# Performance work log

Measured on AMD Instinct MI355X. Metric: run time of the kernel, lower is better.

Reference implementation:

```python
import jax, jax.numpy as jnp
import numpy as np

# FP4 E2M1 value table (codes 0..7 positive, 8..15 negative, sign in MSB)
FP4_VALUES = jnp.array([0.0, 0.5, 1.0, 1.5, 2.0, 3.0, 4.0, 6.0,
                        -0.0, -0.5, -1.0, -1.5, -2.0, -3.0, -4.0, -6.0],
                       dtype=jnp.float32)


def setup_inputs() -> dict:
    key = jax.random.key(0)
    k1, k2, k3, k4 = jax.random.split(key, 4)
    O, I = 4096, 4096
    block = 16
    x = jax.random.normal(k1, (8192, I), dtype=jnp.float32)
    # packed uint4 pairs stored as int32 bytes in [0, 256)
    weight = jax.random.randint(k2, (O, I // 2), 0, 256, dtype=jnp.int32)
    # per-block FP8-style scales (positive)
    weight_scale = jax.random.uniform(k3, (O, I // block), dtype=jnp.float32, minval=0.01, maxval=1.0)
    bias = jax.random.normal(k4, (O,), dtype=jnp.float32)
    return {"x": x, "weight": weight, "weight_scale": weight_scale,
            "bias": bias, "block_size": block}


def _dequant_nvfp4(weight, weight_scale, block_size):
    # unpack two FP4 codes per byte: high nibble is the even (first) element
    hi = (weight >> 4) & 0xF
    lo = weight & 0xF
    O = weight.shape[0]
    codes = jnp.stack([hi, lo], axis=-1).reshape(O, -1)  # [O, I]
    vals = FP4_VALUES[codes]                             # [O, I] f32
    I = vals.shape[1]
    # apply per-block scale
    w = vals.reshape(O, I // block_size, block_size) * weight_scale[:, :, None]
    return w.reshape(O, I)


def reference(x, weight, weight_scale, bias, block_size):
    w = _dequant_nvfp4(weight, weight_scale, block_size)  # [O, I]
    return jnp.einsum('ti,oi->to', x, w) + bias[None, :]
```

## Files before the change

kernel.cpp:

```cpp
#include <hip/hip_runtime.h>
#include <hip/hip_fp16.h>

typedef __attribute__((ext_vector_type(8))) _Float16 f16x8;
typedef __attribute__((ext_vector_type(4))) float f32x4;

#define M_DIM 8192
#define N_DIM 4096
#define K_DIM 4096
#define BM 256
#define BN 256
#define BK 64
#define NT (K_DIM / BK)
#define ITERS (NT / 2)

__constant__ float FP4_LUT[16] = {0.f, 0.5f, 1.f, 1.5f, 2.f, 3.f, 4.f, 6.f,
                                  -0.f, -0.5f, -1.f, -1.5f, -2.f, -3.f, -4.f, -6.f};

__device__ inline void glds16(const void* g, void* l) {
    __builtin_amdgcn_global_load_lds(
        (const __attribute__((address_space(1))) void*)g,
        (__attribute__((address_space(3))) void*)l, 16, 0, 0);
}

__global__ __launch_bounds__(256) void cvt_x_kernel(const float* __restrict__ x,
                                                    _Float16* __restrict__ xh) {
    int i = (blockIdx.x * 256 + threadIdx.x) * 8;
    const float4* p = (const float4*)(x + i);
    float4 a = p[0], b = p[1];
    f16x8 h;
    h[0] = (_Float16)a.x; h[1] = (_Float16)a.y;
    h[2] = (_Float16)a.z; h[3] = (_Float16)a.w;
    h[4] = (_Float16)b.x; h[5] = (_Float16)b.y;
    h[6] = (_Float16)b.z; h[7] = (_Float16)b.w;
    *(f16x8*)(xh + i) = h;
}

__global__ __launch_bounds__(256) void dequant_w_kernel(const int* __restrict__ w,
                                                        const float* __restrict__ wsc,
                                                        _Float16* __restrict__ wh) {
    int t = blockIdx.x * 256 + threadIdx.x;
    int4 b4 = ((const int4*)w)[t];
    int o  = t >> 9;
    int j0 = (t & 511) << 2;
    float s = wsc[(o << 8) + (j0 >> 3)];
    f16x8 h;
    int b;
    b = b4.x; h[0] = (_Float16)(FP4_LUT[(b >> 4) & 15] * s); h[1] = (_Float16)(FP4_LUT[b & 15] * s);
    b = b4.y; h[2] = (_Float16)(FP4_LUT[(b >> 4) & 15] * s); h[3] = (_Float16)(FP4_LUT[b & 15] * s);
    b = b4.z; h[4] = (_Float16)(FP4_LUT[(b >> 4) & 15] * s); h[5] = (_Float16)(FP4_LUT[b & 15] * s);
    b = b4.w; h[6] = (_Float16)(FP4_LUT[(b >> 4) & 15] * s); h[7] = (_Float16)(FP4_LUT[b & 15] * s);
    *(f16x8*)(wh + ((long)o << 12) + (j0 << 1)) = h;
}


#define VM6 asm volatile("s_waitcnt vmcnt(6)" ::: "memory")
#define VM4 asm volatile("s_waitcnt vmcnt(4)" ::: "memory")
#define VM2 asm volatile("s_waitcnt vmcnt(2)" ::: "memory")
#define VM0 asm volatile("s_waitcnt vmcnt(0)" ::: "memory")
#define LG8 asm volatile("s_waitcnt lgkmcnt(8)" ::: "memory")
#define LG4 asm volatile("s_waitcnt lgkmcnt(4)" ::: "memory")
#define LG0 asm volatile("s_waitcnt lgkmcnt(0)" ::: "memory")
#define NOP ((void)0)

#define STAGE(OP, SD, KH, KOFF) do {                                           \
    _Float16* _d = lds + (SD)*32768 + (OP)*16384 + (KH)*8192 + (wid << 9);     \
    const _Float16* _s = ((OP) ? srcB : srcA) + (KOFF);                        \
    glds16(_s, _d);                                                            \
    glds16(_s + (size_t)128 * K_DIM, _d + 4096);                               \
  } while (0)

#define PH(DOAF, NCB, NKH, NMH, AFN, DOBF, BFN, LGW, MHC, AFC, BFC, STG, VMW) do { \
    STG;                                                                       \
    const _Float16* _nb = lds + (NCB)*32768 + (NKH)*8192;                      \
    if (DOAF) {                                                                \
      AFN[0] = *(const f16x8*)(_nb + a_off + (NMH)*2048);                      \
      AFN[1] = *(const f16x8*)(_nb + a_off + (NMH)*2048 + 512);                \
      AFN[2] = *(const f16x8*)(_nb + a_off + (NMH)*2048 + 1024);               \
      AFN[3] = *(const f16x8*)(_nb + a_off + (NMH)*2048 + 1536);               \
    }                                                                          \
    if (DOBF) {                                                                \
      BFN[0] = *(const f16x8*)(_nb + b_off);                                   \
      BFN[1] = *(const f16x8*)(_nb + b_off + 512);                             \
      BFN[2] = *(const f16x8*)(_nb + b_off + 1024);                            \
      BFN[3] = *(const f16x8*)(_nb + b_off + 1536);                            \
    }                                                                          \
    LGW;                                                                       \
    __builtin_amdgcn_s_setprio(1);                                             \
    _Pragma("unroll")                                                          \
    for (int mf = 0; mf < 4; ++mf) {                                           \
      _Pragma("unroll")                                                        \
      for (int nf = 0; nf < 4; ++nf)                                           \
        acc[(MHC)*4 + mf][nf] = __builtin_amdgcn_mfma_f32_16x16x32_f16(        \
            AFC[mf], BFC[nf], acc[(MHC)*4 + mf][nf], 0, 0, 0);                 \
    }                                                                          \
    __builtin_amdgcn_s_setprio(0);                                             \
    VMW;                                                                       \
    __builtin_amdgcn_s_barrier();                                              \
  } while (0)

__global__ __launch_bounds__(512, 2) void gemm_f16_pf(const _Float16* __restrict__ A,
                                                      const _Float16* __restrict__ B,
                                                      const float* __restrict__ bias,
                                                      float* __restrict__ C) {
    __shared__ _Float16 lds[2 * 32768];

    const int tid  = threadIdx.x;
    const int wid  = tid >> 6;
    const int lane = tid & 63;
    const int fr   = lane & 15;
    const int kg   = lane >> 4;
    const int wm   = wid >> 2;
    const int wn   = wid & 3;

    const int c = blockIdx.x & 7;
    const int q = blockIdx.x >> 3;
    const int bm = (c >> 1) * 8 + (q & 7);
    const int bn = (c & 1) * 8 + (q >> 3);
    const int brow = bm * BM;
    const int bcol = bn * BN;

    const int s_col = (((tid & 3) ^ ((tid >> 3) & 3)) << 3);
    const _Float16* srcA = A + (size_t)(brow + (tid >> 2)) * K_DIM + s_col;
    const _Float16* srcB = B + (size_t)(bcol + (tid >> 2)) * K_DIM + s_col;

    const int swz   = ((kg ^ ((fr >> 1) & 3)) << 3);
    const int a_off = (wm * 128 + fr) * 32 + swz;
    const int b_off = 16384 + (wn * 64 + fr) * 32 + swz;

    f16x8 af0[4], af1[4], bf0[4], bf1[4];
    f32x4 acc[8][4] = {};

    STAGE(0, 0, 0, 0);
    STAGE(1, 0, 0, 0);
    STAGE(0, 0, 1, 32);
    STAGE(1, 0, 1, 32);
    STAGE(0, 1, 0, 64);
    STAGE(1, 1, 0, 64);
    VM2;
    __builtin_amdgcn_s_barrier();
    af0[0] = *(const f16x8*)(lds + a_off);
    af0[1] = *(const f16x8*)(lds + a_off + 512);
    af0[2] = *(const f16x8*)(lds + a_off + 1024);
    af0[3] = *(const f16x8*)(lds + a_off + 1536);
    bf0[0] = *(const f16x8*)(lds + b_off);
    bf0[1] = *(const f16x8*)(lds + b_off + 512);
    bf0[2] = *(const f16x8*)(lds + b_off + 1024);
    bf0[3] = *(const f16x8*)(lds + b_off + 1536);

    for (int i = 0; i < ITERS - 1; ++i) {
        const int kb = i << 7;
        PH(1, 0,0,1, af1, 0,bf0, LG4, 0, af0, bf0, STAGE(0,1,1,kb+96),  VM6);
        PH(1, 0,1,0, af0, 1,bf1, LG8, 1, af1, bf0, STAGE(1,1,1,kb+96),  NOP);
        PH(1, 0,1,1, af1, 0,bf0, LG4, 0, af0, bf1, STAGE(0,0,0,kb+128), VM6);
        PH(1, 1,0,0, af0, 1,bf0, LG8, 1, af1, bf1, STAGE(1,0,0,kb+128), NOP);
        PH(1, 1,0,1, af1, 0,bf0, LG4, 0, af0, bf0, STAGE(0,0,1,kb+160), VM6);
        PH(1, 1,1,0, af0, 1,bf1, LG8, 1, af1, bf0, STAGE(1,0,1,kb+160), NOP);
        PH(1, 1,1,1, af1, 0,bf0, LG4, 0, af0, bf1, STAGE(0,1,0,kb+192), VM6);
        PH(1, 0,0,0, af0, 1,bf0, LG8, 1, af1, bf1, STAGE(1,1,0,kb+192), NOP);
    }
    {
        const int kb = (ITERS - 1) << 7;
        PH(1, 0,0,1, af1, 0,bf0, LG4, 0, af0, bf0, STAGE(0,1,1,kb+96), VM6);
        PH(1, 0,1,0, af0, 1,bf1, LG8, 1, af1, bf0, STAGE(1,1,1,kb+96), NOP);
        PH(1, 0,1,1, af1, 0,bf0, LG4, 0, af0, bf1, NOP,                VM4);
        PH(1, 1,0,0, af0, 1,bf0, LG8, 1, af1, bf1, NOP,                NOP);
        PH(1, 1,0,1, af1, 0,bf0, LG4, 0, af0, bf0, NOP,                VM0);
        PH(1, 1,1,0, af0, 1,bf1, LG8, 1, af1, bf0, NOP,                NOP);
        PH(1, 1,1,1, af1, 0,bf0, LG4, 0, af0, bf1, NOP,                NOP);
        PH(0, 0,0,0, af0, 0,bf0, LG0, 1, af1, bf1, NOP,                NOP);
    }

#pragma unroll
    for (int m = 0; m < 8; ++m) {
        int row = brow + wm * 128 + m * 16 + kg * 4;
#pragma unroll
        for (int n = 0; n < 4; ++n) {
            int col = bcol + wn * 64 + n * 16 + fr;
            float bv = bias[col];
#pragma unroll
            for (int j = 0; j < 4; ++j)
                C[(size_t)(row + j) * N_DIM + col] = acc[m][n][j] + bv;
        }
    }
}

__global__ __launch_bounds__(256) void fallback_kernel(const float* __restrict__ x,
                                                       const int* __restrict__ w,
                                                       const float* __restrict__ wsc,
                                                       const float* __restrict__ bias,
                                                       float* __restrict__ out) {
    long idx = (long)blockIdx.x * 256 + threadIdx.x;
    int t = (int)(idx >> 12);
    int o = (int)(idx & 4095);
    float acc = 0.f;
    for (int j = 0; j < K_DIM / 2; ++j) {
        int b = w[o * (K_DIM / 2) + j];
        float s = wsc[(o << 8) + (j >> 3)];
        acc += x[(long)t * K_DIM + 2 * j]     * (FP4_LUT[(b >> 4) & 15] * s);
        acc += x[(long)t * K_DIM + 2 * j + 1] * (FP4_LUT[b & 15] * s);
    }
    out[idx] = acc + bias[o];
}

extern "C" void kernel_launch(void* const* d_in, const int* in_sizes, int n_in,
                              void* d_out, int out_size, void* d_ws, size_t ws_size,
                              hipStream_t stream) {
    const float* x    = (const float*)d_in[0];
    const int*   w    = (const int*)d_in[1];
    const float* wsc  = (const float*)d_in[2];
    const float* bias = (const float*)d_in[3];
    float* out = (float*)d_out;

    const size_t xh_bytes = (size_t)M_DIM * K_DIM * 2;
    const size_t wh_bytes = (size_t)N_DIM * K_DIM * 2;

    if (ws_size >= xh_bytes + wh_bytes) {
        _Float16* xh = (_Float16*)d_ws;
        _Float16* wh = (_Float16*)((char*)d_ws + xh_bytes);
        cvt_x_kernel<<<(M_DIM * K_DIM) / (256 * 8), 256, 0, stream>>>(x, xh);
        dequant_w_kernel<<<(N_DIM * (K_DIM / 2)) / (256 * 4), 256, 0, stream>>>(w, wsc, wh);
        gemm_f16_pf<<<(M_DIM / BM) * (N_DIM / BN), 512, 0, stream>>>(xh, wh, bias, out);
    } else {
        fallback_kernel<<<((long)M_DIM * N_DIM) / 256, 256, 0, stream>>>(x, w, wsc, bias, out);
    }
}
```

Before: 283.2 us.

## Halve workgroup barriers in GEMM main loop by syncing every other phase

```diff
diff --git a/kernel.cpp b/kernel.cpp
--- a/kernel.cpp
+++ b/kernel.cpp
@@ -53,9 +53,7 @@
 }
 
 
-#define VM6 asm volatile("s_waitcnt vmcnt(6)" ::: "memory")
 #define VM4 asm volatile("s_waitcnt vmcnt(4)" ::: "memory")
-#define VM2 asm volatile("s_waitcnt vmcnt(2)" ::: "memory")
 #define VM0 asm volatile("s_waitcnt vmcnt(0)" ::: "memory")
 #define LG8 asm volatile("s_waitcnt lgkmcnt(8)" ::: "memory")
 #define LG4 asm volatile("s_waitcnt lgkmcnt(4)" ::: "memory")
@@ -69,7 +67,7 @@
     glds16(_s + (size_t)128 * K_DIM, _d + 4096);                               \
   } while (0)
 
-#define PH(DOAF, NCB, NKH, NMH, AFN, DOBF, BFN, LGW, MHC, AFC, BFC, STG, VMW) do { \
+#define PH(DOAF, NCB, NKH, NMH, AFN, DOBF, BFN, LGW, MHC, AFC, BFC, STG, VMW, BAR) do { \
     STG;                                                                       \
     const _Float16* _nb = lds + (NCB)*32768 + (NKH)*8192;                      \
     if (DOAF) {                                                                \
@@ -95,7 +93,7 @@
     }                                                                          \
     __builtin_amdgcn_s_setprio(0);                                             \
     VMW;                                                                       \
-    __builtin_amdgcn_s_barrier();                                              \
+    if (BAR) __builtin_amdgcn_s_barrier();                                     \
   } while (0)
 
 __global__ __launch_bounds__(512, 2) void gemm_f16_pf(const _Float16* __restrict__ A,
@@ -136,7 +134,7 @@
     STAGE(1, 0, 1, 32);
     STAGE(0, 1, 0, 64);
     STAGE(1, 1, 0, 64);
-    VM2;
+    VM4;
     __builtin_amdgcn_s_barrier();
     af0[0] = *(const f16x8*)(lds + a_off);
     af0[1] = *(const f16x8*)(lds + a_off + 512);
@@ -149,25 +147,25 @@
 
     for (int i = 0; i < ITERS - 1; ++i) {
         const int kb = i << 7;
-        PH(1, 0,0,1, af1, 0,bf0, LG4, 0, af0, bf0, STAGE(0,1,1,kb+96),  VM6);
-        PH(1, 0,1,0, af0, 1,bf1, LG8, 1, af1, bf0, STAGE(1,1,1,kb+96),  NOP);
-        PH(1, 0,1,1, af1, 0,bf0, LG4, 0, af0, bf1, STAGE(0,0,0,kb+128), VM6);
-        PH(1, 1,0,0, af0, 1,bf0, LG8, 1, af1, bf1, STAGE(1,0,0,kb+128), NOP);
-        PH(1, 1,0,1, af1, 0,bf0, LG4, 0, af0, bf0, STAGE(0,0,1,kb+160), VM6);
-        PH(1, 1,1,0, af0, 1,bf1, LG8, 1, af1, bf0, STAGE(1,0,1,kb+160), NOP);
-        PH(1, 1,1,1, af1, 0,bf0, LG4, 0, af0, bf1, STAGE(0,1,0,kb+192), VM6);
-        PH(1, 0,0,0, af0, 1,bf0, LG8, 1, af1, bf1, STAGE(1,1,0,kb+192), NOP);
+        PH(1, 0,0,1, af1, 0,bf0, LG4, 0, af0, bf0, STAGE(0,1,1,kb+96),  NOP, 0);
+        PH(1, 0,1,0, af0, 1,bf1, LG8, 1, af1, bf0, STAGE(1,1,1,kb+96),  VM4, 1);
+        PH(1, 0,1,1, af1, 0,bf0, LG4, 0, af0, bf1, STAGE(0,0,0,kb+128), NOP, 0);
+        PH(1, 1,0,0, af0, 1,bf0, LG8, 1, af1, bf1, STAGE(1,0,0,kb+128), VM4, 1);
+        PH(1, 1,0,1, af1, 0,bf0, LG4, 0, af0, bf0, STAGE(0,0,1,kb+160), NOP, 0);
+        PH(1, 1,1,0, af0, 1,bf1, LG8, 1, af1, bf0, STAGE(1,0,1,kb+160), VM4, 1);
+        PH(1, 1,1,1, af1, 0,bf0, LG4, 0, af0, bf1, STAGE(0,1,0,kb+192), NOP, 0);
+        PH(1, 0,0,0, af0, 1,bf0, LG8, 1, af1, bf1, STAGE(1,1,0,kb+192), VM4, 1);
     }
     {
         const int kb = (ITERS - 1) << 7;
-        PH(1, 0,0,1, af1, 0,bf0, LG4, 0, af0, bf0, STAGE(0,1,1,kb+96), VM6);
-        PH(1, 0,1,0, af0, 1,bf1, LG8, 1, af1, bf0, STAGE(1,1,1,kb+96), NOP);
-        PH(1, 0,1,1, af1, 0,bf0, LG4, 0, af0, bf1, NOP,                VM4);
-        PH(1, 1,0,0, af0, 1,bf0, LG8, 1, af1, bf1, NOP,                NOP);
-        PH(1, 1,0,1, af1, 0,bf0, LG4, 0, af0, bf0, NOP,                VM0);
-        PH(1, 1,1,0, af0, 1,bf1, LG8, 1, af1, bf0, NOP,                NOP);
-        PH(1, 1,1,1, af1, 0,bf0, LG4, 0, af0, bf1, NOP,                NOP);
-        PH(0, 0,0,0, af0, 0,bf0, LG0, 1, af1, bf1, NOP,                NOP);
+        PH(1, 0,0,1, af1, 0,bf0, LG4, 0, af0, bf0, STAGE(0,1,1,kb+96), NOP, 0);
+        PH(1, 0,1,0, af0, 1,bf1, LG8, 1, af1, bf0, STAGE(1,1,1,kb+96), VM4, 1);
+        PH(1, 0,1,1, af1, 0,bf0, LG4, 0, af0, bf1, NOP,                NOP, 0);
+        PH(1, 1,0,0, af0, 1,bf0, LG8, 1, af1, bf1, NOP,                VM0, 1);
+        PH(1, 1,0,1, af1, 0,bf0, LG4, 0, af0, bf0, NOP,                NOP, 0);
+        PH(1, 1,1,0, af0, 1,bf1, LG8, 1, af1, bf0, NOP,                NOP, 1);
+        PH(1, 1,1,1, af1, 0,bf0, LG4, 0, af0, bf1, NOP,                NOP, 0);
+        PH(0, 0,0,0, af0, 0,bf0, LG0, 1, af1, bf1, NOP,                NOP, 0);
     }
 
 #pragma unroll
```

After: 279.5 us. No clear change (-1.3%).
